# Optimization experiments

Measured on AMD Instinct MI355X. Metric: run time of the kernel, lower is better.

## Reference

```python
import jax, jax.numpy as jnp
import numpy as np

B, C, S = 256, 1024, 14   # batch, channels, spatial (frozen by y.view(b,c,14,14))
C2 = 15                   # channels2 in the module
CAT = C // 2 * 3 + C2     # 1551 = 15 + 512 + 1024
EPS = 1e-5


def _conv(x, w, b, groups, pad):
    out = jax.lax.conv_general_dilated(
        x, w, window_strides=(1, 1), padding=((pad, pad), (pad, pad)),
        dimension_numbers=('NCHW', 'OIHW', 'NCHW'), feature_group_count=groups)
    return out + b[None, :, None, None]


def _bn(x, gamma, beta):
    # training-mode BatchNorm2d: biased batch stats over (N,H,W)
    m = x.mean((0, 2, 3), keepdims=True)
    v = x.var((0, 2, 3), keepdims=True)
    return (x - m) * jax.lax.rsqrt(v + EPS) * gamma[None, :, None, None] + beta[None, :, None, None]


def setup_inputs() -> dict:
    key = jax.random.key(0)
    ks = jax.random.split(key, 16)
    r = C2 // 7  # = 2
    inp = {
        'y': jax.random.normal(ks[0], (B, C2, S * S), jnp.float32),
        'x': jax.random.normal(ks[1], (B, C, S, S), jnp.float32),
        'fc1_w': jax.random.normal(ks[2], (r, C2), jnp.float32) * 0.2,
        'fc2_w': jax.random.normal(ks[3], (C2, r), jnp.float32) * 0.2,
        'conv_w': jax.random.normal(ks[4], (C // 2, C, 1, 1), jnp.float32) * 0.03,
        'conv_b': jnp.zeros((C // 2,), jnp.float32),
        'dconv_w': jax.random.normal(ks[5], (C, 1, 3, 3), jnp.float32) * 0.2,
        'dconv_b': jnp.zeros((C,), jnp.float32),
        'dw1_w': jax.random.normal(ks[6], (CAT, 1, 3, 3), jnp.float32) * 0.2,
        'dw1_b': jnp.zeros((CAT,), jnp.float32),
        'pw1_w': jax.random.normal(ks[7], (C // 2, CAT, 1, 1), jnp.float32) * 0.03,
        'pw1_b': jnp.zeros((C // 2,), jnp.float32),
        'gamma': jnp.ones((C // 2,), jnp.float32),
        'beta': jnp.zeros((C // 2,), jnp.float32),
        'n': 0,
    }
    return inp


def reference(y, x, fc1_w, fc2_w, conv_w, conv_b, dconv_w, dconv_b,
              dw1_w, dw1_b, pw1_w, pw1_b, gamma, beta, n):
    b = y.shape[0]
    y4 = y.reshape(b, C2, S, S)
    # SE block on the 15 sub-channels
    g = y4.mean((2, 3))                              # (b, 15) global avg pool
    h = jax.nn.relu(g @ fc1_w.T) @ fc2_w.T           # (b, 15)
    y1 = y4 * jax.nn.sigmoid(h)[:, :, None, None]
    # depthwise conv on x, then per-(b,c) row covariance of the 14x14 map
    x1 = _conv(x, dconv_w, dconv_b, C, 1)            # (b, C, 14, 14)
    x2 = jax.lax.stop_gradient(x1)                   # .detach() in the original
    xc = x2 - x2.mean(-1, keepdims=True)             # np.cov: rows=vars, cols=obs
    cov = jnp.einsum('bcik,bcjk->bcij', xc, xc) / (S - 1)
    z = _conv(cov, conv_w, conv_b, 1, 0)             # 1x1 conv C -> C//2
    z = jax.nn.sigmoid(_bn(z, gamma, beta))
    for _ in range(n):                               # n=0 at these shapes
        y1 = jax.image.resize(y1, (y1.shape[0], y1.shape[1], y1.shape[2] * 2, y1.shape[3] * 2), 'bilinear')
    cat = jnp.concatenate([y1, z, x], axis=1)        # (b, 1551, 14, 14)
    o = _conv(cat, dw1_w, dw1_b, CAT, 1)             # depthwise 3x3
    o = _conv(o, pw1_w, pw1_b, 1, 0)                 # pointwise 1x1 -> C//2
    return jax.nn.relu(_bn(o, gamma, beta))
```

## Files before the change

kernel.cpp:

```cpp
#include <hip/hip_runtime.h>

typedef unsigned int u32;
typedef unsigned short u16;
typedef __attribute__((ext_vector_type(8))) short bf16x8;
typedef __attribute__((ext_vector_type(4))) float f32x4;
typedef __attribute__((ext_vector_type(4))) u32 u32x4;

#define EPSBN 1e-5f

#define OFF_ADW    0ull
#define OFF_COVT   0ull
#define OFF_S      160563200ull
#define OFF_WBZ    160578560ull
#define OFF_WBP    161627136ull
#define OFF_STATSZ 163265536ull
#define OFF_STATSO 163269632ull
#define OFF_SCZ    163273728ull
#define OFF_SHZ    163275776ull
#define OFF_SCO    163277824ull
#define OFF_SHO    163279872ull

static __device__ __forceinline__ float bf2f(u16 h){
  u32 u = ((u32)h) << 16; float f; __builtin_memcpy(&f, &u, 4); return f;
}
static __device__ __forceinline__ u16 f2bf(float f){
  u32 u; __builtin_memcpy(&u, &f, 4);
  u = (u + 0x7fffu + ((u >> 16) & 1u)) >> 16;
  return (u16)u;
}

__global__ __launch_bounds__(64) void se_kernel(const float* __restrict__ y,
    const float* __restrict__ fc1, const float* __restrict__ fc2, float* __restrict__ sse){
  __shared__ float g[15];
  __shared__ float t[2];
  int b = blockIdx.x, l = threadIdx.x;
  for (int c = 0; c < 15; ++c){
    float p = 0.f;
    for (int k = l; k < 196; k += 64) p += y[((size_t)b*15 + c)*196 + k];
    p += __shfl_xor(p, 32); p += __shfl_xor(p, 16); p += __shfl_xor(p, 8);
    p += __shfl_xor(p, 4);  p += __shfl_xor(p, 2);  p += __shfl_xor(p, 1);
    if (l == 0) g[c] = p * (1.f/196.f);
  }
  __syncthreads();
  if (l < 2){
    float a = 0.f;
    for (int c = 0; c < 15; ++c) a += g[c] * fc1[l*15 + c];
    t[l] = fmaxf(a, 0.f);
  }
  __syncthreads();
  if (l < 15){
    float h = t[0]*fc2[l*2] + t[1]*fc2[l*2+1];
    sse[b*15 + l] = 1.f / (1.f + __expf(-h));
  }
}

__global__ void wconv_kernel(const float* __restrict__ cw, const float* __restrict__ pw,
                             u16* __restrict__ wbz, u16* __restrict__ wbp){
  u32 stride = gridDim.x * blockDim.x;
  for (u32 i = blockIdx.x*blockDim.x + threadIdx.x; i < 524288u; i += stride)
    wbz[i] = f2bf(cw[i]);
  for (u32 i = blockIdx.x*blockDim.x + threadIdx.x; i < 819200u; i += stride){
    u32 n = i / 1600u, k = i - n*1600u;
    wbp[i] = f2bf(k < 1551u ? pw[(size_t)n*1551 + k] : 0.f);
  }
}

static __device__ __forceinline__ void dw3x3_row(const float* __restrict__ m,
    int i, const float* __restrict__ w, float bias, float* __restrict__ ov){
  float r[3][14];
  #pragma unroll
  for (int d = 0; d < 3; ++d){
    int rr = i + d - 1;
    if (rr >= 0 && rr < 14){
      #pragma unroll
      for (int k = 0; k < 14; ++k) r[d][k] = m[rr*14 + k];
    } else {
      #pragma unroll
      for (int k = 0; k < 14; ++k) r[d][k] = 0.f;
    }
  }
  #pragma unroll
  for (int k = 0; k < 14; ++k){
    float a = bias;
    #pragma unroll
    for (int dy = 0; dy < 3; ++dy){
      #pragma unroll
      for (int dx = 0; dx < 3; ++dx){
        int kk = k + dx - 1;
        if (kk >= 0 && kk < 14) a += w[dy*3+dx] * r[dy][kk];
      }
    }
    ov[k] = a;
  }
}

__global__ __launch_bounds__(256,5) void cov_kernel(const float* __restrict__ x,
    const float* __restrict__ dcw, const float* __restrict__ dcb, u16* __restrict__ covT){
  __shared__ __align__(16) float xs[16*324];
  __shared__ __align__(16) u32 xcb[16*132];
  __shared__ float wls[16][9];
  __shared__ float wlb[16];
  u16* covL = (u16*)xs;

  int tid = threadIdx.x;
  int c0 = blockIdx.x * 16, b = blockIdx.y;

  for (int i = tid; i < 1024; i += 256){
    int c = i >> 6, j = i & 63;
    int slot = 0, col = 0;
    bool go = true;
    if (j < 16){ slot = 0; col = j; }
    else if (j < 32){ slot = 15; col = j - 16; }
    else if (j < 46){ slot = j - 31; col = 0; }
    else if (j < 60){ slot = j - 45; col = 15; }
    else go = false;
    if (go) xs[c*324 + slot*20 + col] = 0.f;
  }
  {
    const float4* xg = (const float4*)(x + ((size_t)b*1024 + c0)*196);
    for (int i = tid; i < 784; i += 256){
      float4 v = xg[i];
      u32 c = (u32)i / 49u, p0 = ((u32)i - c*49u)*4u;
      #pragma unroll
      for (int e = 0; e < 4; ++e){
        u32 p = p0 + e;
        u32 row = p / 14u, col = p - row*14u;
        float vv = (e==0)?v.x:(e==1)?v.y:(e==2)?v.z:v.w;
        xs[c*324u + (row+1u)*20u + (col+1u)] = vv;
      }
    }
  }
  if (tid < 144) wls[tid/9][tid%9] = dcw[(size_t)(c0 + tid/9)*9 + (tid%9)];
  if (tid < 16) wlb[tid] = dcb[c0 + tid];
  __syncthreads();

  {
    int c = tid >> 4, i = tid & 15;
    u32 q[8];
    #pragma unroll
    for (int j = 0; j < 8; ++j) q[j] = 0u;
    if (i < 14){
      float wreg[9];
      #pragma unroll
      for (int qq = 0; qq < 9; ++qq) wreg[qq] = wls[c][qq];
      float bb = wlb[c];
      const float4* base = (const float4*)xs;
      float rr[3][16];
      #pragma unroll
      for (int d = 0; d < 3; ++d)
        #pragma unroll
        for (int j = 0; j < 4; ++j)
          *(float4*)&rr[d][j*4] = base[c*81 + (i + d)*5 + j];
      float ov[14];
      #pragma unroll
      for (int k = 0; k < 14; ++k){
        float a = bb;
        #pragma unroll
        for (int dy = 0; dy < 3; ++dy)
          #pragma unroll
          for (int dx = 0; dx < 3; ++dx)
            a += wreg[dy*3+dx] * rr[dy][k + dx];
        ov[k] = a;
      }
      float mean = 0.f;
      #pragma unroll
      for (int k = 0; k < 14; ++k) mean += ov[k];
      mean *= (1.f/14.f);
      #pragma unroll
      for (int j = 0; j < 7; ++j){
        u32 lo = f2bf(ov[2*j]   - mean);
        u32 hi = f2bf(ov[2*j+1] - mean);
        q[j] = lo | (hi << 16);
      }
    }
    u32x4 q0 = {q[0], q[1], q[2], q[3]};
    u32x4 q1 = {q[4], q[5], q[6], q[7]};
    *(u32x4*)&xcb[c*132 + i*8]     = q0;
    *(u32x4*)&xcb[c*132 + i*8 + 4] = q1;
  }
  __syncthreads();

  {
    int w = tid >> 6, l = tid & 63, lr = l & 15, lq = l >> 4;
    #pragma unroll
    for (int cc = 0; cc < 4; ++cc){
      int c = w*4 + cc;
      bf16x8 a = {0,0,0,0,0,0,0,0};
      if (lq < 2) a = *(const bf16x8*)&xcb[c*132 + lr*8 + lq*4];
      f32x4 d = {0.f,0.f,0.f,0.f};
      d = __builtin_amdgcn_mfma_f32_16x16x32_bf16(a, a, d, 0, 0, 0);
      if (lr < 14){
        #pragma unroll
        for (int r = 0; r < 4; ++r){
          int rowi = lq*4 + r;
          if (rowi < 14) covL[c*210 + rowi*14 + lr] = f2bf(d[r] * (1.f/13.f));
        }
      }
    }
  }
  __syncthreads();

  for (int i = tid; i < 1568; i += 256){
    int cp = i & 7, ij = i >> 3;
    u32 v0 = covL[(2*cp)*210 + ij];
    u32 v1 = covL[(2*cp+1)*210 + ij];
    *(u32*)(covT + ((size_t)(b*196 + ij)*1024 + c0 + 2*cp)) = v0 | (v1 << 16);
  }
}

__global__ __launch_bounds__(256,5) void adw_kernel(
    const float* __restrict__ y, const float* __restrict__ sse,
    const u16* __restrict__ zraw, const float* __restrict__ scz, const float* __restrict__ shz,
    const float* __restrict__ x, const float* __restrict__ dw1w, const float* __restrict__ dw1b,
    u16* __restrict__ Adw){
  __shared__ __align__(16) float ms[32*201 + 4];
  __shared__ float wd[32][9];
  __shared__ float bd[32];
  int tid = threadIdx.x;
  int cc0 = blockIdx.x * 32, b = blockIdx.y;

  for (int i = tid; i < 288; i += 256){
    int c = i / 9, q = i - c*9;
    int cc = cc0 + c;
    wd[c][q] = (cc < 1551) ? dw1w[(size_t)cc*9 + q] : 0.f;
  }
  if (tid < 32) bd[tid] = (cc0 + tid < 1551) ? dw1b[cc0 + tid] : 0.f;

  if (cc0 < 15){
    int ny = 15 - cc0; if (ny > 32) ny = 32;
    for (int i = tid; i < ny*196; i += 256){
      u32 c = (u32)i / 196u, p = (u32)i - c*196u;
      int cc = cc0 + (int)c;
      ms[c*201u + p] = y[((size_t)b*15 + cc)*196 + p] * sse[b*15 + cc];
    }
  }
  {
    int zs = cc0 > 15 ? cc0 : 15;
    int ze = cc0 + 32 < 527 ? cc0 + 32 : 527;
    if (zs < ze){
      int nz = ze - zs, lbase = zs - cc0, obase = zs - 15;
      for (int i = tid; i < nz*196; i += 256){
        int oo = i % nz, p = i / nz;
        int o = obase + oo;
        float v = bf2f(zraw[((size_t)b*196 + p)*512 + o]);
        v = v * scz[o] + shz[o];
        v = 1.f / (1.f + __expf(-v));
        ms[(u32)(lbase + oo)*201u + p] = v;
      }
    }
  }
  {
    int xs_ = cc0 > 527 ? cc0 : 527;
    int xe = cc0 + 32 < 1551 ? cc0 + 32 : 1551;
    if (xs_ < xe){
      int nx = xe - xs_, lbase = xs_ - cc0, cxs = xs_ - 527;
      for (int i = tid; i < nx*196; i += 256){
        u32 c = (u32)i / 196u, p = (u32)i - c*196u;
        ms[(u32)(lbase + (int)c)*201u + p] = x[((size_t)b*1024 + cxs + c)*196 + p];
      }
    }
  }
  {
    int ps = cc0 > 1551 ? cc0 : 1551;
    int pe = cc0 + 32;
    if (ps < pe){
      int np = pe - ps, lbase = ps - cc0;
      for (int i = tid; i < np*196; i += 256){
        u32 c = (u32)i / 196u, p = (u32)i - c*196u;
        ms[(u32)(lbase + (int)c)*201u + p] = 0.f;
      }
    }
  }
  __syncthreads();

  for (int t = tid; t < 448; t += 256){
    int cc = t & 31, i = t >> 5;
    float ov[14];
    dw3x3_row(&ms[cc*201], i, &wd[cc][0], bd[cc], ov);
    size_t obase = ((size_t)b*196 + i*14) * 1600 + cc0 + cc;
    #pragma unroll
    for (int k = 0; k < 14; ++k) Adw[obase + (size_t)k*1600] = f2bf(ov[k]);
  }
}

template<int MODE>
__global__ __launch_bounds__(256,2) void gemm_kernel(
    const u16* __restrict__ A, const u16* __restrict__ Bw,
    const float* __restrict__ bias, void* __restrict__ outp,
    float* __restrict__ stats, int K){
  __shared__ __align__(16) char smem[33280];
  u16* As = (u16*)smem;
  u16* Bs = (u16*)(smem + 16384);

  int tid = threadIdx.x;
  int w = tid >> 6, l = tid & 63;
  int wm = w >> 1, wn = w & 1;
  int lr = l & 15, lq = l >> 4;
  int m0 = blockIdx.y * 128;
  int n0 = blockIdx.x * 128;

  f32x4 acc[4][4] = {};
  int kTiles = K >> 6;

  for (int kt = 0; kt < kTiles; ++kt){
    bf16x8 av[4], bv[4];
    #pragma unroll
    for (int i = 0; i < 4; ++i){
      int s = tid + i*256;
      int row = s >> 3, c8 = s & 7, sc = c8 ^ (row & 7);
      av[i] = *(const bf16x8*)(A  + (size_t)(m0 + row)*K + kt*64 + sc*8);
      bv[i] = *(const bf16x8*)(Bw + (size_t)(n0 + row)*K + kt*64 + sc*8);
    }
    __syncthreads();
    #pragma unroll
    for (int i = 0; i < 4; ++i){
      int s = tid + i*256;
      int row = s >> 3, c8 = s & 7;
      *(bf16x8*)(As + row*64 + c8*8) = av[i];
      *(bf16x8*)(Bs + row*64 + c8*8) = bv[i];
    }
    __syncthreads();
    #pragma unroll
    for (int ks = 0; ks < 2; ++ks){
      bf16x8 af[4], bfv[4];
      #pragma unroll
      for (int mi = 0; mi < 4; ++mi){
        int row = wm*64 + mi*16 + lr;
        int q = (ks*4 + lq) ^ (row & 7);
        af[mi] = *(const bf16x8*)(As + row*64 + q*8);
      }
      #pragma unroll
      for (int ni = 0; ni < 4; ++ni){
        int row = wn*64 + ni*16 + lr;
        int q = (ks*4 + lq) ^ (row & 7);
        bfv[ni] = *(const bf16x8*)(Bs + row*64 + q*8);
      }
      #pragma unroll
      for (int mi = 0; mi < 4; ++mi)
        #pragma unroll
        for (int ni = 0; ni < 4; ++ni)
          acc[mi][ni] = __builtin_amdgcn_mfma_f32_16x16x32_bf16(af[mi], bfv[ni], acc[mi][ni], 0, 0, 0);
    }
  }

  #pragma unroll
  for (int ni = 0; ni < 4; ++ni){
    int col = n0 + wn*64 + ni*16 + lr;
    float bb = bias[col];
    float s1 = 0.f, s2 = 0.f;
    #pragma unroll
    for (int mi = 0; mi < 4; ++mi)
      #pragma unroll
      for (int r = 0; r < 4; ++r){
        float v = acc[mi][ni][r] + bb;
        acc[mi][ni][r] = v;
        s1 += v; s2 += v*v;
      }
    s1 += __shfl_xor(s1, 16); s1 += __shfl_xor(s1, 32);
    s2 += __shfl_xor(s2, 16); s2 += __shfl_xor(s2, 32);
    if (lq == 0){
      atomicAdd(&stats[col], s1);
      atomicAdd(&stats[512 + col], s2);
    }
  }

  if (MODE == 0){
    u16* zo = (u16*)outp;
    #pragma unroll
    for (int mi = 0; mi < 4; ++mi)
      #pragma unroll
      for (int r = 0; r < 4; ++r){
        int m = m0 + wm*64 + mi*16 + lq*4 + r;
        size_t base = (size_t)m*512 + n0 + wn*64 + lr;
        #pragma unroll
        for (int ni = 0; ni < 4; ++ni)
          zo[base + ni*16] = f2bf(acc[mi][ni][r]);
      }
  } else {
    __syncthreads();
    float* eb = (float*)smem;
    #pragma unroll
    for (int rnd = 0; rnd < 2; ++rnd){
      if (wm == rnd){
        float* e = eb + wn * (64*65);
        #pragma unroll
        for (int mi = 0; mi < 4; ++mi)
          #pragma unroll
          for (int ni = 0; ni < 4; ++ni)
            #pragma unroll
            for (int r = 0; r < 4; ++r)
              e[(mi*16 + lq*4 + r)*65 + ni*16 + lr] = acc[mi][ni][r];
        int m = m0 + wm*64 + l;
        u32 bq = (u32)m / 196u;
        u32 ij = (u32)m - bq*196u;
        float* ob = (float*)outp + ((size_t)bq*512 + n0 + wn*64)*196 + ij;
        #pragma unroll 8
        for (int no = 0; no < 64; ++no)
          ob[(size_t)no*196] = e[l*65 + no];
      }
      __syncthreads();
    }
  }
}

__global__ void bnprep_kernel(const float* __restrict__ stats, const float* __restrict__ gamma,
    const float* __restrict__ beta, float* __restrict__ sc, float* __restrict__ sh){
  int o = threadIdx.x;
  float m = stats[o] * (1.f/50176.f);
  float v = stats[512+o] * (1.f/50176.f) - m*m;
  float inv = rsqrtf(v + EPSBN);
  float g = gamma[o] * inv;
  sc[o] = g;
  sh[o] = beta[o] - m*g;
}

__global__ void final_kernel(float4* __restrict__ o4, const float* __restrict__ sc,
                             const float* __restrict__ sh){
  u32 stride = gridDim.x * blockDim.x;
  for (u32 i = blockIdx.x*blockDim.x + threadIdx.x; i < 6422528u; i += stride){
    u32 oc = (i / 49u) & 511u;
    float s = sc[oc], t = sh[oc];
    float4 v = o4[i];
    v.x = fmaxf(fmaf(v.x, s, t), 0.f);
    v.y = fmaxf(fmaf(v.y, s, t), 0.f);
    v.z = fmaxf(fmaf(v.z, s, t), 0.f);
    v.w = fmaxf(fmaf(v.w, s, t), 0.f);
    o4[i] = v;
  }
}

extern "C" void kernel_launch(void* const* d_in, const int* in_sizes, int n_in,
                              void* d_out, int out_size, void* d_ws, size_t ws_size,
                              hipStream_t stream){
  (void)in_sizes; (void)n_in; (void)out_size; (void)ws_size;
  const float* y      = (const float*)d_in[0];
  const float* x      = (const float*)d_in[1];
  const float* fc1    = (const float*)d_in[2];
  const float* fc2    = (const float*)d_in[3];
  const float* convw  = (const float*)d_in[4];
  const float* convb  = (const float*)d_in[5];
  const float* dconvw = (const float*)d_in[6];
  const float* dconvb = (const float*)d_in[7];
  const float* dw1w   = (const float*)d_in[8];
  const float* dw1b   = (const float*)d_in[9];
  const float* pw1w   = (const float*)d_in[10];
  const float* pw1b   = (const float*)d_in[11];
  const float* gamma  = (const float*)d_in[12];
  const float* beta   = (const float*)d_in[13];

  char* ws = (char*)d_ws;
  u16* covT   = (u16*)(ws + OFF_COVT);
  u16* Adw    = (u16*)(ws + OFF_ADW);
  float* sse  = (float*)(ws + OFF_S);
  u16* wbz    = (u16*)(ws + OFF_WBZ);
  u16* wbp    = (u16*)(ws + OFF_WBP);
  float* statsZ = (float*)(ws + OFF_STATSZ);
  float* statsO = (float*)(ws + OFF_STATSO);
  float* scz  = (float*)(ws + OFF_SCZ);
  float* shz  = (float*)(ws + OFF_SHZ);
  float* sco  = (float*)(ws + OFF_SCO);
  float* sho  = (float*)(ws + OFF_SHO);
  u16* zraw   = (u16*)d_out;
  float* outf = (float*)d_out;

  hipMemsetAsync(statsZ, 0, 8192, stream);
  se_kernel<<<256, 64, 0, stream>>>(y, fc1, fc2, sse);
  wconv_kernel<<<2048, 256, 0, stream>>>(convw, pw1w, wbz, wbp);
  cov_kernel<<<dim3(64, 256), 256, 0, stream>>>(x, dconvw, dconvb, covT);
  gemm_kernel<0><<<dim3(4, 392), 256, 0, stream>>>(covT, wbz, convb, (void*)zraw, statsZ, 1024);
  bnprep_kernel<<<1, 512, 0, stream>>>(statsZ, gamma, beta, scz, shz);
  adw_kernel<<<dim3(50, 256), 256, 0, stream>>>(y, sse, zraw, scz, shz, x, dw1w, dw1b, Adw);
  gemm_kernel<1><<<dim3(4, 392), 256, 0, stream>>>(Adw, wbp, pw1b, (void*)outf, statsO, 1600);
  bnprep_kernel<<<1, 512, 0, stream>>>(statsO, gamma, beta, sco, sho);
  final_kernel<<<8192, 256, 0, stream>>>((float4*)outf, sco, sho);
}
```

Baseline: 547.9 us.

## Load GEMM tiles directly to LDS and simplify cov kernel halo handling

The GEMM kernel now uses global_load_lds (direct global-to-LDS 16-byte loads) instead of staging through registers, and raises the occupancy hint from 2 to 3 blocks per CU. The aim is fewer VGPRs and no separate LDS write pass. The cov kernel drops its zero-padded halo layout: it stores rows contiguously, clamps row indices and masks the boundary weights, which cuts the halo zeroing and scalar scatter. It also packs channel pairs into u32 covariance stores. The direct-to-LDS path only works if the builtin's per-lane addressing matches the swizzled layout, and it removes the register prefetch overlap.

```diff
diff --git a/kernel.cpp b/kernel.cpp
--- a/kernel.cpp
+++ b/kernel.cpp
@@ -7,6 +7,10 @@
 typedef __attribute__((ext_vector_type(4))) u32 u32x4;
 
 #define EPSBN 1e-5f
+
+#define GLDS16(gp, lp) __builtin_amdgcn_global_load_lds( \
+    (const __attribute__((address_space(1))) u32*)(gp), \
+    (__attribute__((address_space(3))) u32*)(lp), 16, 0, 0)
 
 #define OFF_ADW    0ull
 #define OFF_COVT   0ull
@@ -96,38 +100,21 @@
 
 __global__ __launch_bounds__(256,5) void cov_kernel(const float* __restrict__ x,
     const float* __restrict__ dcw, const float* __restrict__ dcb, u16* __restrict__ covT){
-  __shared__ __align__(16) float xs[16*324];
+  __shared__ __align__(16) float xs[16*200];
   __shared__ __align__(16) u32 xcb[16*132];
   __shared__ float wls[16][9];
   __shared__ float wlb[16];
-  u16* covL = (u16*)xs;
+  u32* covL32 = (u32*)xs;
 
   int tid = threadIdx.x;
   int c0 = blockIdx.x * 16, b = blockIdx.y;
 
-  for (int i = tid; i < 1024; i += 256){
-    int c = i >> 6, j = i & 63;
-    int slot = 0, col = 0;
-    bool go = true;
-    if (j < 16){ slot = 0; col = j; }
-    else if (j < 32){ slot = 15; col = j - 16; }
-    else if (j < 46){ slot = j - 31; col = 0; }
-    else if (j < 60){ slot = j - 45; col = 15; }
-    else go = false;
-    if (go) xs[c*324 + slot*20 + col] = 0.f;
-  }
   {
     const float4* xg = (const float4*)(x + ((size_t)b*1024 + c0)*196);
     for (int i = tid; i < 784; i += 256){
       float4 v = xg[i];
-      u32 c = (u32)i / 49u, p0 = ((u32)i - c*49u)*4u;
-      #pragma unroll
-      for (int e = 0; e < 4; ++e){
-        u32 p = p0 + e;
-        u32 row = p / 14u, col = p - row*14u;
-        float vv = (e==0)?v.x:(e==1)?v.y:(e==2)?v.z:v.w;
-        xs[c*324u + (row+1u)*20u + (col+1u)] = vv;
-      }
+      u32 c = (u32)i / 49u, p4 = (u32)i - c*49u;
+      *(float4*)&xs[c*200u + p4*4u] = v;
     }
   }
   if (tid < 144) wls[tid/9][tid%9] = dcw[(size_t)(c0 + tid/9)*9 + (tid%9)];
@@ -140,17 +127,24 @@
     #pragma unroll
     for (int j = 0; j < 8; ++j) q[j] = 0u;
     if (i < 14){
-      float wreg[9];
-      #pragma unroll
-      for (int qq = 0; qq < 9; ++qq) wreg[qq] = wls[c][qq];
+      float wr[9];
+      #pragma unroll
+      for (int qq = 0; qq < 9; ++qq) wr[qq] = wls[c][qq];
+      float topm = (i > 0) ? 1.f : 0.f, botm = (i < 13) ? 1.f : 0.f;
+      wr[0] *= topm; wr[1] *= topm; wr[2] *= topm;
+      wr[6] *= botm; wr[7] *= botm; wr[8] *= botm;
       float bb = wlb[c];
-      const float4* base = (const float4*)xs;
       float rr[3][16];
       #pragma unroll
-      for (int d = 0; d < 3; ++d)
-        #pragma unroll
-        for (int j = 0; j < 4; ++j)
-          *(float4*)&rr[d][j*4] = base[c*81 + (i + d)*5 + j];
+      for (int d = 0; d < 3; ++d){
+        rr[d][0] = 0.f; rr[d][15] = 0.f;
+        int rowr = i + d - 1;
+        rowr = rowr < 0 ? 0 : (rowr > 13 ? 13 : rowr);
+        const float* src = &xs[c*200 + rowr*14];
+        #pragma unroll
+        for (int j = 0; j < 7; ++j)
+          *(float2*)&rr[d][1 + 2*j] = *(const float2*)&src[2*j];
+      }
       float ov[14];
       #pragma unroll
       for (int k = 0; k < 14; ++k){
@@ -159,7 +153,7 @@
         for (int dy = 0; dy < 3; ++dy)
           #pragma unroll
           for (int dx = 0; dx < 3; ++dx)
-            a += wreg[dy*3+dx] * rr[dy][k + dx];
+            a += wr[dy*3+dx] * rr[dy][k + dx];
         ov[k] = a;
       }
       float mean = 0.f;
@@ -183,17 +177,25 @@
   {
     int w = tid >> 6, l = tid & 63, lr = l & 15, lq = l >> 4;
     #pragma unroll
-    for (int cc = 0; cc < 4; ++cc){
-      int c = w*4 + cc;
-      bf16x8 a = {0,0,0,0,0,0,0,0};
-      if (lq < 2) a = *(const bf16x8*)&xcb[c*132 + lr*8 + lq*4];
-      f32x4 d = {0.f,0.f,0.f,0.f};
-      d = __builtin_amdgcn_mfma_f32_16x16x32_bf16(a, a, d, 0, 0, 0);
+    for (int pp = 0; pp < 2; ++pp){
+      int clo = w*4 + 2*pp;
+      bf16x8 alo = {0,0,0,0,0,0,0,0}, ahi = {0,0,0,0,0,0,0,0};
+      if (lq < 2){
+        alo = *(const bf16x8*)&xcb[clo*132 + lr*8 + lq*4];
+        ahi = *(const bf16x8*)&xcb[(clo+1)*132 + lr*8 + lq*4];
+      }
+      f32x4 dlo = {0.f,0.f,0.f,0.f}, dhi = {0.f,0.f,0.f,0.f};
+      dlo = __builtin_amdgcn_mfma_f32_16x16x32_bf16(alo, alo, dlo, 0, 0, 0);
+      dhi = __builtin_amdgcn_mfma_f32_16x16x32_bf16(ahi, ahi, dhi, 0, 0, 0);
       if (lr < 14){
+        int cp = w*2 + pp;
         #pragma unroll
         for (int r = 0; r < 4; ++r){
           int rowi = lq*4 + r;
-          if (rowi < 14) covL[c*210 + rowi*14 + lr] = f2bf(d[r] * (1.f/13.f));
+          if (rowi < 14){
+            u32 vv = (u32)f2bf(dlo[r] * (1.f/13.f)) | ((u32)f2bf(dhi[r] * (1.f/13.f)) << 16);
+            covL32[cp*210 + rowi*14 + lr] = vv;
+          }
         }
       }
     }
@@ -202,9 +204,8 @@
 
   for (int i = tid; i < 1568; i += 256){
     int cp = i & 7, ij = i >> 3;
-    u32 v0 = covL[(2*cp)*210 + ij];
-    u32 v1 = covL[(2*cp+1)*210 + ij];
-    *(u32*)(covT + ((size_t)(b*196 + ij)*1024 + c0 + 2*cp)) = v0 | (v1 << 16);
+    u32 v = covL32[cp*210 + ij];
+    *(u32*)(covT + ((size_t)(b*196 + ij)*1024 + c0 + 2*cp)) = v;
   }
 }
 
@@ -284,7 +285,7 @@
 }
 
 template<int MODE>
-__global__ __launch_bounds__(256,2) void gemm_kernel(
+__global__ __launch_bounds__(256,3) void gemm_kernel(
     const u16* __restrict__ A, const u16* __restrict__ Bw,
     const float* __restrict__ bias, void* __restrict__ outp,
     float* __restrict__ stats, int K){
@@ -303,21 +304,13 @@
   int kTiles = K >> 6;
 
   for (int kt = 0; kt < kTiles; ++kt){
-    bf16x8 av[4], bv[4];
+    if (kt) __syncthreads();
     #pragma unroll
     for (int i = 0; i < 4; ++i){
       int s = tid + i*256;
       int row = s >> 3, c8 = s & 7, sc = c8 ^ (row & 7);
-      av[i] = *(const bf16x8*)(A  + (size_t)(m0 + row)*K + kt*64 + sc*8);
-      bv[i] = *(const bf16x8*)(Bw + (size_t)(n0 + row)*K + kt*64 + sc*8);
-    }
-    __syncthreads();
-    #pragma unroll
-    for (int i = 0; i < 4; ++i){
-      int s = tid + i*256;
-      int row = s >> 3, c8 = s & 7;
-      *(bf16x8*)(As + row*64 + c8*8) = av[i];
-      *(bf16x8*)(Bs + row*64 + c8*8) = bv[i];
+      GLDS16(A  + (size_t)(m0 + row)*K + kt*64 + sc*8, As + s*8);
+      GLDS16(Bw + (size_t)(n0 + row)*K + kt*64 + sc*8, Bs + s*8);
     }
     __syncthreads();
     #pragma unroll
```

Result: no change. 542.1 us (-1.1%).
